# Kernel tuning notes

Hardware: AMD Instinct MI355X
Metric: run time of the kernel (lower is better)

## Reference

```python
import jax, jax.numpy as jnp
import numpy as np

N_LVL = 127.0   # 8-bit symmetric: 2**(8-1) - 1
BN_EPS = 1e-5
PATCH = 16


def quant_act(x):
    """Per-tensor 8-bit symmetric quant-dequant (HAWQ-style QuantAct, dynamic range)."""
    scale = jnp.max(jnp.abs(x)) / N_LVL
    xq = jnp.clip(jnp.round(x / scale), -N_LVL, N_LVL) * scale
    return xq, scale


def setup_inputs() -> dict:
    key = jax.random.key(0)
    k0, k1, k2, k3, k4 = jax.random.split(key, 5)
    B, C, H = 128, 3, 224
    dim = 768
    x = jax.random.normal(k0, (B, C, H, H), jnp.float32)
    W = jax.random.normal(k1, (dim, C, PATCH, PATCH), jnp.float32) * 0.02
    b = jax.random.normal(k2, (dim,), jnp.float32) * 0.02
    gamma = jnp.ones((dim,), jnp.float32)
    beta = jnp.zeros((dim,), jnp.float32)
    run_mean = jax.random.normal(k3, (dim,), jnp.float32) * 0.1
    run_var = jax.random.uniform(k4, (dim,), jnp.float32, 0.5, 1.5)
    return {"x": x, "W": W, "b": b, "gamma": gamma, "beta": beta,
            "run_mean": run_mean, "run_var": run_var}


def reference(x, W, b, gamma, beta, run_mean, run_var):
    # --- quant_input ---
    x_q, pre_s = quant_act(x)                                   # [B,3,224,224], scalar
    # --- QuantConv2d: per-out-channel 8-bit symmetric weight quant ---
    w_scale = jnp.max(jnp.abs(W), axis=(1, 2, 3), keepdims=True) / N_LVL  # [dim,1,1,1]
    w_int = jnp.round(W / w_scale)
    x_int = x_q / pre_s                                         # integer-valued activations
    comb_s = w_scale[:, 0, 0, 0] * pre_s                        # [dim] conv output scale
    b_int = jnp.round(b / comb_s)
    y = jax.lax.conv_general_dilated(
        x_int, w_int, window_strides=(PATCH, PATCH), padding='VALID',
        dimension_numbers=('NCHW', 'OIHW', 'NCHW'))             # [B,768,14,14]
    y = (y + b_int[None, :, None, None]) * comb_s[None, :, None, None]
    # --- quant_act_conv ---
    y, _ = quant_act(y)
    # --- GELU (torch nn.GELU default: exact erf) ---
    y = jax.nn.gelu(y, approximate=False)
    # --- qact1 ---
    y, _ = quant_act(y)
    # --- BatchNorm2d (eval mode, running stats) ---
    inv = gamma / jnp.sqrt(run_var + BN_EPS)
    y = y * inv[None, :, None, None] + (beta - run_mean * inv)[None, :, None, None]
    # --- qact2 ---
    y, act_scale = quant_act(y)
    return y, act_scale
```

## Files before the change

kernel.cpp:

```cpp
#include <hip/hip_runtime.h>

#define TOT   19267584
#define MROWS 25088
#define KD    768
#define NPB   196
#define CHW   150528

typedef unsigned int uint;
typedef __attribute__((ext_vector_type(4))) int i32x4;

#define OFF_AQ   0ull
#define OFF_WQ   19267584ull
#define OFF_WSC  19857408ull
#define OFF_INV  19860480ull
#define OFF_SHF  19863552ull
#define OFF_PA   19866624ull
#define OFF_PB   19871328ull
#define OFF_SC   19876032ull
#define OFF_PMN  19886880ull
#define OFF_PMX  24703776ull
#define OFF_PM2  19267584ull
#define OFF_PX2  19316736ull

__device__ __forceinline__ float wave_max(float v) {
#pragma unroll
  for (int off = 32; off > 0; off >>= 1) v = fmaxf(v, __shfl_xor(v, off));
  return v;
}

__device__ __forceinline__ float block_max(float v) {
  __shared__ float red[4];
  v = wave_max(v);
  __syncthreads();
  if ((threadIdx.x & 63) == 0) red[threadIdx.x >> 6] = v;
  __syncthreads();
  return fmaxf(fmaxf(red[0], red[1]), fmaxf(red[2], red[3]));
}

__device__ __forceinline__ size_t tiled_addr(int row, int k) {
  return (size_t)(row >> 7) * 98304 + (size_t)(k >> 6) * 8192 + ((row & 127) << 6) + (k & 63);
}

__global__ void k_max_wq(const float* __restrict__ x, float* __restrict__ pA,
                         const float* __restrict__ W, const float* __restrict__ gamma,
                         const float* __restrict__ beta, const float* __restrict__ rmean,
                         const float* __restrict__ rvar, signed char* __restrict__ wq,
                         float* __restrict__ wscale, float* __restrict__ inv_,
                         float* __restrict__ shf) {
  if (blockIdx.x < 1176) {
    const int i0 = blockIdx.x * 256 + threadIdx.x;
    const float4* x4 = (const float4*)x;
    float m = 0.f;
#pragma unroll
    for (int j = 0; j < 16; j += 4) {
      float4 a = x4[i0 + (j + 0) * 301056];
      float4 b = x4[i0 + (j + 1) * 301056];
      float4 c = x4[i0 + (j + 2) * 301056];
      float4 d = x4[i0 + (j + 3) * 301056];
      m = fmaxf(m, fmaxf(fmaxf(fabsf(a.x), fabsf(a.y)), fmaxf(fabsf(a.z), fabsf(a.w))));
      m = fmaxf(m, fmaxf(fmaxf(fabsf(b.x), fabsf(b.y)), fmaxf(fabsf(b.z), fabsf(b.w))));
      m = fmaxf(m, fmaxf(fmaxf(fabsf(c.x), fabsf(c.y)), fmaxf(fabsf(c.z), fabsf(c.w))));
      m = fmaxf(m, fmaxf(fmaxf(fabsf(d.x), fabsf(d.y)), fmaxf(fabsf(d.z), fabsf(d.w))));
    }
    float bm = block_max(m);
    if (threadIdx.x == 0) pA[blockIdx.x] = bm;
  } else {
    const int oc = blockIdx.x - 1176;
    const float* row = W + oc * KD;
    float m = 0.f;
    for (int k = threadIdx.x; k < KD; k += 256) m = fmaxf(m, fabsf(row[k]));
    const float ws_ = block_max(m) / 127.0f;
    for (int k = threadIdx.x; k < KD; k += 256)
      wq[tiled_addr(oc, k)] = (signed char)(int)rintf(row[k] / ws_);
    if (threadIdx.x == 0) {
      wscale[oc] = ws_;
      float iv = gamma[oc] / sqrtf(rvar[oc] + 1e-5f);
      inv_[oc] = iv;
      shf[oc] = __fsub_rn(beta[oc], __fmul_rn(rmean[oc], iv));
    }
  }
}

__global__ void k_im2col(const float* __restrict__ x, const float* __restrict__ pA,
                         signed char* __restrict__ aq) {
  float mm = 0.f;
  for (int i = threadIdx.x; i < 1176; i += 256) mm = fmaxf(mm, pA[i]);
  const float ps = block_max(mm) / 127.0f;
  const int u = blockIdx.x * 256 + threadIdx.x;
  const int p = u / 48, r = u - p * 48;
  const int c = r >> 4, kh = r & 15;
  const int b = p / NPB, pp = p - b * NPB;
  const int ph = pp / 14, pw = pp - ph * 14;
  const float* src = x + (((b * 3 + c) * 224 + ph * 16 + kh) * 224 + pw * 16);
  float4 v0 = *(const float4*)(src);
  float4 v1 = *(const float4*)(src + 4);
  float4 v2 = *(const float4*)(src + 8);
  float4 v3 = *(const float4*)(src + 12);
#define Q8(v) ((int)fminf(fmaxf(rintf((v) / ps), -127.f), 127.f) & 255)
  uint4 o;
  o.x = Q8(v0.x) | (Q8(v0.y) << 8) | (Q8(v0.z) << 16) | ((uint)Q8(v0.w) << 24);
  o.y = Q8(v1.x) | (Q8(v1.y) << 8) | (Q8(v1.z) << 16) | ((uint)Q8(v1.w) << 24);
  o.z = Q8(v2.x) | (Q8(v2.y) << 8) | (Q8(v2.z) << 16) | ((uint)Q8(v2.w) << 24);
  o.w = Q8(v3.x) | (Q8(v3.y) << 8) | (Q8(v3.z) << 16) | ((uint)Q8(v3.w) << 24);
#undef Q8
  *(uint4*)(aq + (size_t)(p >> 7) * 98304 + (size_t)(r >> 2) * 8192 + ((p & 127) << 6) +
            ((r & 3) << 4)) = o;
}

__device__ __forceinline__ void gl_lds16(const void* g, void* l) {
  __builtin_amdgcn_global_load_lds((const __attribute__((address_space(1))) void*)g,
                                   (__attribute__((address_space(3))) void*)l, 16, 0, 0);
}

__global__ __launch_bounds__(256) void k_gemm(const signed char* __restrict__ aq,
                                              const signed char* __restrict__ wq,
                                              const float* __restrict__ bias,
                                              const float* __restrict__ wscale,
                                              const float* __restrict__ pA,
                                              float* __restrict__ y,
                                              float* __restrict__ pB) {
  __shared__ __align__(16) signed char lA[2][8192];
  __shared__ __align__(16) signed char lB[2][8192];
  const int tid = threadIdx.x, lane = tid & 63, wv = tid >> 6;
  const int bsw = (blockIdx.x & 7) * 147 + (blockIdx.x >> 3);
  const int bm = bsw / 6, bn = bsw - 6 * (bsw / 6);
  const int wr = wv >> 1, wc = wv & 1;

  float mm = 0.f;
  for (int i = tid; i < 1176; i += 256) mm = fmaxf(mm, pA[i]);
  const float ps_ = block_max(mm) / 127.0f;

  const int ci0 = wv * 2, ci1 = wv * 2 + 1;
  const int lo = ((lane >> 2) << 6) + (((lane & 3) ^ ((lane >> 3) & 3)) << 4);
  const signed char* gA0 = aq + (size_t)bm * 98304 + ci0 * 1024 + lo;
  const signed char* gA1 = aq + (size_t)bm * 98304 + ci1 * 1024 + lo;
  const signed char* gB0 = wq + (size_t)bn * 98304 + ci0 * 1024 + lo;
  const signed char* gB1 = wq + (size_t)bn * 98304 + ci1 * 1024 + lo;

  i32x4 acc[4][4];
#pragma unroll
  for (int m = 0; m < 4; ++m)
#pragma unroll
    for (int n = 0; n < 4; ++n) acc[m][n] = (i32x4){0, 0, 0, 0};

  const int rbase = lane & 15;
  const int kg = ((lane >> 4) << 4) ^ (((lane >> 1) & 3) << 4);

#define STAGE(T, B)                                   \
  {                                                   \
    const size_t kk_ = (size_t)(T) * 8192;            \
    gl_lds16(gA0 + kk_, &lA[B][ci0 * 1024]);          \
    gl_lds16(gA1 + kk_, &lA[B][ci1 * 1024]);          \
    gl_lds16(gB0 + kk_, &lB[B][ci0 * 1024]);          \
    gl_lds16(gB1 + kk_, &lB[B][ci1 * 1024]);          \
  }

  STAGE(0, 0)
  __syncthreads();

  int cur = 0;
  for (int t = 0; t < 12; ++t) {
    if (t < 11) STAGE(t + 1, cur ^ 1)
    i32x4 af[4], bfr[4];
#pragma unroll
    for (int m = 0; m < 4; ++m)
      af[m] = *(const i32x4*)&lA[cur][(wr * 64 + m * 16 + rbase) * 64 + kg];
#pragma unroll
    for (int n = 0; n < 4; ++n)
      bfr[n] = *(const i32x4*)&lB[cur][(wc * 64 + n * 16 + rbase) * 64 + kg];
#pragma unroll
    for (int m = 0; m < 4; ++m)
#pragma unroll
      for (int n = 0; n < 4; ++n)
        acc[m][n] = __builtin_amdgcn_mfma_i32_16x16x64_i8(bfr[n], af[m], acc[m][n], 0, 0, 0);
    __syncthreads();
    cur ^= 1;
  }
#undef STAGE

  float lmax = 0.f;
#pragma unroll
  for (int n = 0; n < 4; ++n) {
    const int ocb = bn * 128 + wc * 64 + n * 16 + ((lane >> 4) << 2);
    const float4 ws4 = *(const float4*)&wscale[ocb];
    const float4 b4 = *(const float4*)&bias[ocb];
    const float c0 = ws4.x * ps_, c1 = ws4.y * ps_, c2 = ws4.z * ps_, c3 = ws4.w * ps_;
    const float i0 = rintf(b4.x / c0), i1 = rintf(b4.y / c1);
    const float i2 = rintf(b4.z / c2), i3 = rintf(b4.w / c3);
#pragma unroll
    for (int m = 0; m < 4; ++m) {
      const int p = bm * 128 + wr * 64 + m * 16 + rbase;
      float4 o;
      o.x = ((float)acc[m][n][0] + i0) * c0;
      o.y = ((float)acc[m][n][1] + i1) * c1;
      o.z = ((float)acc[m][n][2] + i2) * c2;
      o.w = ((float)acc[m][n][3] + i3) * c3;
      lmax = fmaxf(lmax, fmaxf(fmaxf(fabsf(o.x), fabsf(o.y)), fmaxf(fabsf(o.z), fabsf(o.w))));
      *(float4*)(y + (size_t)p * 768 + ocb) = o;
    }
  }
  float bm_ = block_max(lmax);
  if (tid == 0) pB[blockIdx.x] = bm_;
}

__global__ void k_gelu(const float* __restrict__ y, const float* __restrict__ pB,
                       signed char* __restrict__ k1, float* __restrict__ pmn,
                       float* __restrict__ pmx) {
  const int b = blockIdx.x;
  const int t = threadIdx.x;
  __shared__ float red[3];
  __shared__ float tab[255];
  float mm = 0.f;
  for (int i = t; i < 1176; i += 192) mm = fmaxf(mm, pB[i]);
  mm = wave_max(mm);
  __syncthreads();
  if ((t & 63) == 0) red[t >> 6] = mm;
  __syncthreads();
  const float s1 = fmaxf(fmaxf(red[0], red[1]), red[2]) / 127.0f;
  for (int i = t; i < 255; i += 192) {
    float y1 = (float)(i - 127) * s1;
    float e = erff(y1 * 0.70710678118654752f);
    tab[i] = (y1 * (e + 1.0f)) * 0.5f;
  }
  __syncthreads();
  float mn0 = 1e30f, mx0 = -1e30f, mn1 = 1e30f, mx1 = -1e30f;
  float mn2 = 1e30f, mx2 = -1e30f, mn3 = 1e30f, mx3 = -1e30f;
  const float4* y4 = (const float4*)y + (size_t)b * 16 * 192 + t;
  char4* k4 = (char4*)k1 + (size_t)b * 16 * 192 + t;
#pragma unroll 4
  for (int row = 0; row < 16; ++row) {
    float4 v = y4[row * 192];
    int a = (int)fminf(fmaxf(rintf(v.x / s1), -127.f), 127.f);
    int bq = (int)fminf(fmaxf(rintf(v.y / s1), -127.f), 127.f);
    int cq = (int)fminf(fmaxf(rintf(v.z / s1), -127.f), 127.f);
    int dq = (int)fminf(fmaxf(rintf(v.w / s1), -127.f), 127.f);
    char4 kk;
    kk.x = (signed char)a; kk.y = (signed char)bq;
    kk.z = (signed char)cq; kk.w = (signed char)dq;
    k4[row * 192] = kk;
    float g0 = tab[a + 127], g1 = tab[bq + 127], g2 = tab[cq + 127], g3 = tab[dq + 127];
    mn0 = fminf(mn0, g0); mx0 = fmaxf(mx0, g0);
    mn1 = fminf(mn1, g1); mx1 = fmaxf(mx1, g1);
    mn2 = fminf(mn2, g2); mx2 = fmaxf(mx2, g2);
    mn3 = fminf(mn3, g3); mx3 = fmaxf(mx3, g3);
  }
  float4 omn, omx;
  omn.x = mn0; omn.y = mn1; omn.z = mn2; omn.w = mn3;
  omx.x = mx0; omx.y = mx1; omx.z = mx2; omx.w = mx3;
  ((float4*)pmn)[(size_t)b * 192 + t] = omn;
  ((float4*)pmx)[(size_t)b * 192 + t] = omx;
}

__global__ void k_chred(const float* __restrict__ pmn, const float* __restrict__ pmx,
                        float* __restrict__ pm2, float* __restrict__ px2) {
  const int cg = blockIdx.x % 12, rc = blockIdx.x / 12;
  const int lane = threadIdx.x & 63, wv = threadIdx.x >> 6;
  const int c = cg * 64 + lane;
  float lo = 1e30f, hi = -1e30f;
  for (int i = wv; i < 98; i += 4) {
    const size_t a = (size_t)(rc * 98 + i) * 768 + c;
    lo = fminf(lo, pmn[a]);
    hi = fmaxf(hi, pmx[a]);
  }
  __shared__ float smn[4][64], smx[4][64];
  smn[wv][lane] = lo;
  smx[wv][lane] = hi;
  __syncthreads();
  if (threadIdx.x < 64) {
    float l = fminf(fminf(smn[0][lane], smn[1][lane]), fminf(smn[2][lane], smn[3][lane]));
    float h = fmaxf(fmaxf(smx[0][lane], smx[1][lane]), fmaxf(smx[2][lane], smx[3][lane]));
    pm2[rc * 768 + c] = l;
    px2[rc * 768 + c] = h;
  }
}

__global__ void k_scales(const float* __restrict__ pB, const float* __restrict__ pm2,
                         const float* __restrict__ px2, const float* __restrict__ inv_,
                         const float* __restrict__ shf, uint* __restrict__ sc) {
  const int t = threadIdx.x;
  float m = 0.f;
  for (int i = t; i < 1176; i += 256) m = fmaxf(m, pB[i]);
  const float s1 = block_max(m) / 127.0f;
  float cmn[3], cmx[3];
  float m2 = 0.f;
#pragma unroll
  for (int ci = 0; ci < 3; ++ci) {
    const int c = t + ci * 256;
    float mn = 1e30f, mx = -1e30f;
#pragma unroll
    for (int r = 0; r < 16; ++r) {
      mn = fminf(mn, pm2[r * 768 + c]);
      mx = fmaxf(mx, px2[r * 768 + c]);
    }
    cmn[ci] = mn;
    cmx[ci] = mx;
    m2 = fmaxf(m2, fmaxf(fabsf(mn), fabsf(mx)));
  }
  const float s2 = block_max(m2) / 127.0f;
  float m4 = 0.f;
#pragma unroll
  for (int ci = 0; ci < 3; ++ci) {
    const int c = t + ci * 256;
    float iv = inv_[c], sh = shf[c];
    float a = fminf(fmaxf(rintf(cmn[ci] / s2), -127.f), 127.f) * s2;
    float b = fminf(fmaxf(rintf(cmx[ci] / s2), -127.f), 127.f) * s2;
    float ya = __fadd_rn(__fmul_rn(a, iv), sh);
    float yb = __fadd_rn(__fmul_rn(b, iv), sh);
    m4 = fmaxf(m4, fmaxf(fabsf(ya), fabsf(yb)));
  }
  const float s3 = block_max(m4) / 127.0f;
  if (t == 0) {
    sc[0] = __float_as_uint(s1);
    sc[1] = __float_as_uint(s2);
    sc[2] = __float_as_uint(s3);
  }
}

__global__ __launch_bounds__(256) void k_final(const signed char* __restrict__ k1,
                                               const uint* __restrict__ sc,
                                               const float* __restrict__ inv_,
                                               const float* __restrict__ shf,
                                               float* __restrict__ out) {
  __shared__ signed char ks[49 * 772];
  __shared__ float tab[255];
  const float s1 = __uint_as_float(sc[0]);
  const float s2 = __uint_as_float(sc[1]);
  const float s3 = __uint_as_float(sc[2]);
  const int t = threadIdx.x;
  for (int i = t; i < 255; i += 256) {
    float y1 = (float)(i - 127) * s1;
    float e = erff(y1 * 0.70710678118654752f);
    float y2 = (y1 * (e + 1.0f)) * 0.5f;
    float q2 = fminf(fmaxf(rintf(y2 / s2), -127.f), 127.f);
    tab[i] = q2 * s2;
  }
  const int img = blockIdx.x >> 2, ch = blockIdx.x & 3;
  const int q0 = ch * 49;
  const uint4* src = (const uint4*)(k1 + (size_t)img * 150528 + (size_t)q0 * 768);
  for (int i = t; i < 2352; i += 256) {
    uint4 v = src[i];
    const int q = i / 48, r = i - q * 48;
    *(uint4*)&ks[q * 772 + r * 16] = v;
  }
  __syncthreads();
  const int lane = t & 63, wv = t >> 6;
  float* ob = out + (size_t)img * CHW + q0 + lane;
  if (lane < 49) {
    const signed char* kcol = &ks[lane * 772];
    for (int j = 0; j < 192; ++j) {
      const int oc = wv * 192 + j;
      const float iv = inv_[oc], sh = shf[oc];
      const int a = kcol[oc];
      const float f = __fadd_rn(__fmul_rn(tab[a + 127], iv), sh);
      ob[(size_t)oc * 196] = fminf(fmaxf(rintf(f / s3), -127.f), 127.f) * s3;
    }
  }
  if (blockIdx.x == 0 && t == 0) out[TOT] = s3;
}

extern "C" void kernel_launch(void* const* d_in, const int* in_sizes, int n_in,
                              void* d_out, int out_size, void* d_ws, size_t ws_size,
                              hipStream_t stream) {
  const float* x     = (const float*)d_in[0];
  const float* W     = (const float*)d_in[1];
  const float* bias  = (const float*)d_in[2];
  const float* gamma = (const float*)d_in[3];
  const float* beta  = (const float*)d_in[4];
  const float* rmean = (const float*)d_in[5];
  const float* rvar  = (const float*)d_in[6];
  float* out = (float*)d_out;
  char* ws = (char*)d_ws;

  signed char* aq  = (signed char*)(ws + OFF_AQ);
  signed char* wq  = (signed char*)(ws + OFF_WQ);
  float* wsc  = (float*)(ws + OFF_WSC);
  float* inv_ = (float*)(ws + OFF_INV);
  float* shf  = (float*)(ws + OFF_SHF);
  float* pA   = (float*)(ws + OFF_PA);
  float* pB   = (float*)(ws + OFF_PB);
  uint*  sc   = (uint*)(ws + OFF_SC);
  float* pmn  = (float*)(ws + OFF_PMN);
  float* pmx  = (float*)(ws + OFF_PMX);
  float* pm2  = (float*)(ws + OFF_PM2);
  float* px2  = (float*)(ws + OFF_PX2);
  signed char* k1 = (signed char*)(ws + OFF_AQ);

  k_max_wq<<<1944, 256, 0, stream>>>(x, pA, W, gamma, beta, rmean, rvar, wq, wsc, inv_, shf);
  k_im2col<<<4704, 256, 0, stream>>>(x, pA, aq);
  k_gemm<<<1176, 256, 0, stream>>>(aq, wq, bias, wsc, pA, out, pB);
  k_gelu<<<1568, 192, 0, stream>>>(out, pB, k1, pmn, pmx);
  k_chred<<<192, 256, 0, stream>>>(pmn, pmx, pm2, px2);
  k_scales<<<1, 256, 0, stream>>>(pB, pm2, px2, inv_, shf, sc);
  k_final<<<512, 256, 0, stream>>>(k1, sc, inv_, shf, out);
}
```

Measured before the change: 140.0 us.

## Triple-buffer GEMM LDS pipeline and pass input scale from im2col

The int8 GEMM moves from a two-stage to a three-stage global-to-LDS pipeline. It uses explicit vmcnt waits and a single barrier per k-step, so loads stay two stages ahead of the MFMA work. The GEMM also reads the input quantization scale from a workspace slot written by im2col, instead of re-reducing 1176 partial maxima in every block. LDS usage grows, which may reduce occupancy, and correctness relies on the hand-written waitcnt counts.

```diff
diff --git a/kernel.cpp b/kernel.cpp
--- a/kernel.cpp
+++ b/kernel.cpp
@@ -82,10 +82,11 @@
 }
 
 __global__ void k_im2col(const float* __restrict__ x, const float* __restrict__ pA,
-                         signed char* __restrict__ aq) {
+                         signed char* __restrict__ aq, uint* __restrict__ sc) {
   float mm = 0.f;
   for (int i = threadIdx.x; i < 1176; i += 256) mm = fmaxf(mm, pA[i]);
   const float ps = block_max(mm) / 127.0f;
+  if (blockIdx.x == 0 && threadIdx.x == 0) sc[3] = __float_as_uint(ps);
   const int u = blockIdx.x * 256 + threadIdx.x;
   const int p = u / 48, r = u - p * 48;
   const int c = r >> 4, kh = r & 15;
@@ -116,19 +117,16 @@
                                               const signed char* __restrict__ wq,
                                               const float* __restrict__ bias,
                                               const float* __restrict__ wscale,
-                                              const float* __restrict__ pA,
+                                              const uint* __restrict__ sc,
                                               float* __restrict__ y,
                                               float* __restrict__ pB) {
-  __shared__ __align__(16) signed char lA[2][8192];
-  __shared__ __align__(16) signed char lB[2][8192];
+  __shared__ __align__(16) signed char lA[3][8192];
+  __shared__ __align__(16) signed char lB[3][8192];
   const int tid = threadIdx.x, lane = tid & 63, wv = tid >> 6;
   const int bsw = (blockIdx.x & 7) * 147 + (blockIdx.x >> 3);
   const int bm = bsw / 6, bn = bsw - 6 * (bsw / 6);
   const int wr = wv >> 1, wc = wv & 1;
-
-  float mm = 0.f;
-  for (int i = tid; i < 1176; i += 256) mm = fmaxf(mm, pA[i]);
-  const float ps_ = block_max(mm) / 127.0f;
+  const float ps_ = __uint_as_float(sc[3]);
 
   const int ci0 = wv * 2, ci1 = wv * 2 + 1;
   const int lo = ((lane >> 2) << 6) + (((lane & 3) ^ ((lane >> 3) & 3)) << 4);
@@ -156,25 +154,27 @@
   }
 
   STAGE(0, 0)
-  __syncthreads();
-
-  int cur = 0;
+  STAGE(1, 1)
+#pragma unroll
   for (int t = 0; t < 12; ++t) {
-    if (t < 11) STAGE(t + 1, cur ^ 1)
+    if (t < 11) { asm volatile("s_waitcnt vmcnt(4)" ::: "memory"); }
+    else        { asm volatile("s_waitcnt vmcnt(0)" ::: "memory"); }
+    __builtin_amdgcn_s_barrier();
+    __builtin_amdgcn_sched_barrier(0);
+    const int b = t % 3;
     i32x4 af[4], bfr[4];
 #pragma unroll
     for (int m = 0; m < 4; ++m)
-      af[m] = *(const i32x4*)&lA[cur][(wr * 64 + m * 16 + rbase) * 64 + kg];
+      af[m] = *(const i32x4*)&lA[b][(wr * 64 + m * 16 + rbase) * 64 + kg];
 #pragma unroll
     for (int n = 0; n < 4; ++n)
-      bfr[n] = *(const i32x4*)&lB[cur][(wc * 64 + n * 16 + rbase) * 64 + kg];
+      bfr[n] = *(const i32x4*)&lB[b][(wc * 64 + n * 16 + rbase) * 64 + kg];
+    if (t < 10) STAGE(t + 2, (t + 2) % 3)
 #pragma unroll
     for (int m = 0; m < 4; ++m)
 #pragma unroll
       for (int n = 0; n < 4; ++n)
         acc[m][n] = __builtin_amdgcn_mfma_i32_16x16x64_i8(bfr[n], af[m], acc[m][n], 0, 0, 0);
-    __syncthreads();
-    cur ^= 1;
   }
 #undef STAGE
 
@@ -386,8 +386,8 @@
   signed char* k1 = (signed char*)(ws + OFF_AQ);
 
   k_max_wq<<<1944, 256, 0, stream>>>(x, pA, W, gamma, beta, rmean, rvar, wq, wsc, inv_, shf);
-  k_im2col<<<4704, 256, 0, stream>>>(x, pA, aq);
-  k_gemm<<<1176, 256, 0, stream>>>(aq, wq, bias, wsc, pA, out, pB);
+  k_im2col<<<4704, 256, 0, stream>>>(x, pA, aq, sc);
+  k_gemm<<<1176, 256, 0, stream>>>(aq, wq, bias, wsc, sc, out, pB);
   k_gelu<<<1568, 192, 0, stream>>>(out, pB, k1, pmn, pmx);
   k_chred<<<192, 256, 0, stream>>>(pmn, pmx, pm2, px2);
   k_scales<<<1, 256, 0, stream>>>(pB, pm2, px2, inv_, shf, sc);
```

Result: no change. 140.3 us (+0.2%).

## Recompute GEMM twice to avoid fp32 intermediate round-trip; fuse GELU quant into GEMM

Applied to the files above, without the earlier changes.

The conv GEMM is split into two passes. The first pass only computes the global abs-max of the conv output. The second pass recomputes the GEMM and directly emits the int8 quantized activations plus per-channel GELU min/max, replacing the separate GELU kernel. This removes the 77MB fp32 write and re-read of the intermediate output at the cost of running the int8 GEMM twice. The activation scale is now broadcast through a scalar slot, and the channel reduction sizes are adjusted for the new partial layout.

```diff
diff --git a/kernel.cpp b/kernel.cpp
--- a/kernel.cpp
+++ b/kernel.cpp
@@ -17,10 +17,11 @@
 #define OFF_PA   19866624ull
 #define OFF_PB   19871328ull
 #define OFF_SC   19876032ull
-#define OFF_PMN  19886880ull
-#define OFF_PMX  24703776ull
-#define OFF_PM2  19267584ull
-#define OFF_PX2  19316736ull
+#define OFF_K1   19876864ull
+#define OFF_PMN  39144448ull
+#define OFF_PMX  39746560ull
+#define OFF_PM2  40348672ull
+#define OFF_PX2  40391680ull
 
 __device__ __forceinline__ float wave_max(float v) {
 #pragma unroll
@@ -82,10 +83,11 @@
 }
 
 __global__ void k_im2col(const float* __restrict__ x, const float* __restrict__ pA,
-                         signed char* __restrict__ aq) {
+                         signed char* __restrict__ aq, uint* __restrict__ sc) {
   float mm = 0.f;
   for (int i = threadIdx.x; i < 1176; i += 256) mm = fmaxf(mm, pA[i]);
   const float ps = block_max(mm) / 127.0f;
+  if (blockIdx.x == 0 && threadIdx.x == 0) sc[3] = __float_as_uint(ps);
   const int u = blockIdx.x * 256 + threadIdx.x;
   const int p = u / 48, r = u - p * 48;
   const int c = r >> 4, kh = r & 15;
@@ -112,23 +114,18 @@
                                    (__attribute__((address_space(3))) void*)l, 16, 0, 0);
 }
 
-__global__ __launch_bounds__(256) void k_gemm(const signed char* __restrict__ aq,
-                                              const signed char* __restrict__ wq,
-                                              const float* __restrict__ bias,
-                                              const float* __restrict__ wscale,
-                                              const float* __restrict__ pA,
-                                              float* __restrict__ y,
-                                              float* __restrict__ pB) {
+__global__ __launch_bounds__(256) void k_gemm_max(const signed char* __restrict__ aq,
+                                                  const signed char* __restrict__ wq,
+                                                  const float* __restrict__ bias,
+                                                  const float* __restrict__ wscale,
+                                                  const uint* __restrict__ sc,
+                                                  float* __restrict__ pB) {
   __shared__ __align__(16) signed char lA[2][8192];
   __shared__ __align__(16) signed char lB[2][8192];
   const int tid = threadIdx.x, lane = tid & 63, wv = tid >> 6;
   const int bsw = (blockIdx.x & 7) * 147 + (blockIdx.x >> 3);
   const int bm = bsw / 6, bn = bsw - 6 * (bsw / 6);
   const int wr = wv >> 1, wc = wv & 1;
-
-  float mm = 0.f;
-  for (int i = tid; i < 1176; i += 256) mm = fmaxf(mm, pA[i]);
-  const float ps_ = block_max(mm) / 127.0f;
 
   const int ci0 = wv * 2, ci1 = wv * 2 + 1;
   const int lo = ((lane >> 2) << 6) + (((lane & 3) ^ ((lane >> 3) & 3)) << 4);
@@ -154,10 +151,8 @@
     gl_lds16(gB0 + kk_, &lB[B][ci0 * 1024]);          \
     gl_lds16(gB1 + kk_, &lB[B][ci1 * 1024]);          \
   }
-
   STAGE(0, 0)
   __syncthreads();
-
   int cur = 0;
   for (int t = 0; t < 12; ++t) {
     if (t < 11) STAGE(t + 1, cur ^ 1)
@@ -178,6 +173,7 @@
   }
 #undef STAGE
 
+  const float ps_ = __uint_as_float(sc[3]);
   float lmax = 0.f;
 #pragma unroll
   for (int n = 0; n < 4; ++n) {
@@ -189,66 +185,146 @@
     const float i2 = rintf(b4.z / c2), i3 = rintf(b4.w / c3);
 #pragma unroll
     for (int m = 0; m < 4; ++m) {
-      const int p = bm * 128 + wr * 64 + m * 16 + rbase;
-      float4 o;
-      o.x = ((float)acc[m][n][0] + i0) * c0;
-      o.y = ((float)acc[m][n][1] + i1) * c1;
-      o.z = ((float)acc[m][n][2] + i2) * c2;
-      o.w = ((float)acc[m][n][3] + i3) * c3;
-      lmax = fmaxf(lmax, fmaxf(fmaxf(fabsf(o.x), fabsf(o.y)), fmaxf(fabsf(o.z), fabsf(o.w))));
-      *(float4*)(y + (size_t)p * 768 + ocb) = o;
+      float ox = ((float)acc[m][n][0] + i0) * c0;
+      float oy = ((float)acc[m][n][1] + i1) * c1;
+      float oz = ((float)acc[m][n][2] + i2) * c2;
+      float ow = ((float)acc[m][n][3] + i3) * c3;
+      lmax = fmaxf(lmax, fmaxf(fmaxf(fabsf(ox), fabsf(oy)), fmaxf(fabsf(oz), fabsf(ow))));
     }
   }
   float bm_ = block_max(lmax);
   if (tid == 0) pB[blockIdx.x] = bm_;
 }
 
-__global__ void k_gelu(const float* __restrict__ y, const float* __restrict__ pB,
-                       signed char* __restrict__ k1, float* __restrict__ pmn,
-                       float* __restrict__ pmx) {
-  const int b = blockIdx.x;
-  const int t = threadIdx.x;
-  __shared__ float red[3];
+__global__ __launch_bounds__(256) void k_gemm_k1(const signed char* __restrict__ aq,
+                                                 const signed char* __restrict__ wq,
+                                                 const float* __restrict__ bias,
+                                                 const float* __restrict__ wscale,
+                                                 const uint* __restrict__ sc,
+                                                 const float* __restrict__ pB,
+                                                 signed char* __restrict__ k1,
+                                                 float* __restrict__ pmn,
+                                                 float* __restrict__ pmx) {
+  __shared__ __align__(16) signed char lA[2][8192];
+  __shared__ __align__(16) signed char lB[2][8192];
   __shared__ float tab[255];
+  __shared__ float smnf[2][2][4][4][4], smxf[2][2][4][4][4];
+  const int tid = threadIdx.x, lane = tid & 63, wv = tid >> 6;
+  const int bsw = (blockIdx.x & 7) * 147 + (blockIdx.x >> 3);
+  const int bm = bsw / 6, bn = bsw - 6 * (bsw / 6);
+  const int wr = wv >> 1, wc = wv & 1;
+
   float mm = 0.f;
-  for (int i = t; i < 1176; i += 192) mm = fmaxf(mm, pB[i]);
-  mm = wave_max(mm);
-  __syncthreads();
-  if ((t & 63) == 0) red[t >> 6] = mm;
-  __syncthreads();
-  const float s1 = fmaxf(fmaxf(red[0], red[1]), red[2]) / 127.0f;
-  for (int i = t; i < 255; i += 192) {
+  for (int i = tid; i < 1176; i += 256) mm = fmaxf(mm, pB[i]);
+  const float s1 = block_max(mm) / 127.0f;
+  for (int i = tid; i < 255; i += 256) {
     float y1 = (float)(i - 127) * s1;
     float e = erff(y1 * 0.70710678118654752f);
     tab[i] = (y1 * (e + 1.0f)) * 0.5f;
   }
-  __syncthreads();
-  float mn0 = 1e30f, mx0 = -1e30f, mn1 = 1e30f, mx1 = -1e30f;
-  float mn2 = 1e30f, mx2 = -1e30f, mn3 = 1e30f, mx3 = -1e30f;
-  const float4* y4 = (const float4*)y + (size_t)b * 16 * 192 + t;
-  char4* k4 = (char4*)k1 + (size_t)b * 16 * 192 + t;
-#pragma unroll 4
-  for (int row = 0; row < 16; ++row) {
-    float4 v = y4[row * 192];
-    int a = (int)fminf(fmaxf(rintf(v.x / s1), -127.f), 127.f);
-    int bq = (int)fminf(fmaxf(rintf(v.y / s1), -127.f), 127.f);
-    int cq = (int)fminf(fmaxf(rintf(v.z / s1), -127.f), 127.f);
-    int dq = (int)fminf(fmaxf(rintf(v.w / s1), -127.f), 127.f);
-    char4 kk;
-    kk.x = (signed char)a; kk.y = (signed char)bq;
-    kk.z = (signed char)cq; kk.w = (signed char)dq;
-    k4[row * 192] = kk;
-    float g0 = tab[a + 127], g1 = tab[bq + 127], g2 = tab[cq + 127], g3 = tab[dq + 127];
-    mn0 = fminf(mn0, g0); mx0 = fmaxf(mx0, g0);
-    mn1 = fminf(mn1, g1); mx1 = fmaxf(mx1, g1);
-    mn2 = fminf(mn2, g2); mx2 = fmaxf(mx2, g2);
-    mn3 = fminf(mn3, g3); mx3 = fmaxf(mx3, g3);
-  }
-  float4 omn, omx;
-  omn.x = mn0; omn.y = mn1; omn.z = mn2; omn.w = mn3;
-  omx.x = mx0; omx.y = mx1; omx.z = mx2; omx.w = mx3;
-  ((float4*)pmn)[(size_t)b * 192 + t] = omn;
-  ((float4*)pmx)[(size_t)b * 192 + t] = omx;
+
+  const int ci0 = wv * 2, ci1 = wv * 2 + 1;
+  const int lo = ((lane >> 2) << 6) + (((lane & 3) ^ ((lane >> 3) & 3)) << 4);
+  const signed char* gA0 = aq + (size_t)bm * 98304 + ci0 * 1024 + lo;
+  const signed char* gA1 = aq + (size_t)bm * 98304 + ci1 * 1024 + lo;
+  const signed char* gB0 = wq + (size_t)bn * 98304 + ci0 * 1024 + lo;
+  const signed char* gB1 = wq + (size_t)bn * 98304 + ci1 * 1024 + lo;
+
+  i32x4 acc[4][4];
+#pragma unroll
+  for (int m = 0; m < 4; ++m)
+#pragma unroll
+    for (int n = 0; n < 4; ++n) acc[m][n] = (i32x4){0, 0, 0, 0};
+
+  const int rbase = lane & 15;
+  const int kg = ((lane >> 4) << 4) ^ (((lane >> 1) & 3) << 4);
+
+#define STAGE(T, B)                                   \
+  {                                                   \
+    const size_t kk_ = (size_t)(T) * 8192;            \
+    gl_lds16(gA0 + kk_, &lA[B][ci0 * 1024]);          \
+    gl_lds16(gA1 + kk_, &lA[B][ci1 * 1024]);          \
+    gl_lds16(gB0 + kk_, &lB[B][ci0 * 1024]);          \
+    gl_lds16(gB1 + kk_, &lB[B][ci1 * 1024]);          \
+  }
+  STAGE(0, 0)
+  __syncthreads();
+  int cur = 0;
+  for (int t = 0; t < 12; ++t) {
+    if (t < 11) STAGE(t + 1, cur ^ 1)
+    i32x4 af[4], bfr[4];
+#pragma unroll
+    for (int m = 0; m < 4; ++m)
+      af[m] = *(const i32x4*)&lA[cur][(wr * 64 + m * 16 + rbase) * 64 + kg];
+#pragma unroll
+    for (int n = 0; n < 4; ++n)
+      bfr[n] = *(const i32x4*)&lB[cur][(wc * 64 + n * 16 + rbase) * 64 + kg];
+#pragma unroll
+    for (int m = 0; m < 4; ++m)
+#pragma unroll
+      for (int n = 0; n < 4; ++n)
+        acc[m][n] = __builtin_amdgcn_mfma_i32_16x16x64_i8(bfr[n], af[m], acc[m][n], 0, 0, 0);
+    __syncthreads();
+    cur ^= 1;
+  }
+#undef STAGE
+
+  const float ps_ = __uint_as_float(sc[3]);
+  const int g = lane >> 4;
+#pragma unroll
+  for (int n = 0; n < 4; ++n) {
+    const int ocb = bn * 128 + wc * 64 + n * 16 + (g << 2);
+    const float4 ws4 = *(const float4*)&wscale[ocb];
+    const float4 b4 = *(const float4*)&bias[ocb];
+    const float c0 = ws4.x * ps_, c1 = ws4.y * ps_, c2 = ws4.z * ps_, c3 = ws4.w * ps_;
+    const float i0 = rintf(b4.x / c0), i1 = rintf(b4.y / c1);
+    const float i2 = rintf(b4.z / c2), i3 = rintf(b4.w / c3);
+    float jmn0 = 1e30f, jmn1 = 1e30f, jmn2 = 1e30f, jmn3 = 1e30f;
+    float jmx0 = -1e30f, jmx1 = -1e30f, jmx2 = -1e30f, jmx3 = -1e30f;
+#pragma unroll
+    for (int m = 0; m < 4; ++m) {
+      const int p = bm * 128 + wr * 64 + m * 16 + rbase;
+      float ox = ((float)acc[m][n][0] + i0) * c0;
+      float oy = ((float)acc[m][n][1] + i1) * c1;
+      float oz = ((float)acc[m][n][2] + i2) * c2;
+      float ow = ((float)acc[m][n][3] + i3) * c3;
+      int q0 = (int)fminf(fmaxf(rintf(ox / s1), -127.f), 127.f);
+      int q1 = (int)fminf(fmaxf(rintf(oy / s1), -127.f), 127.f);
+      int q2 = (int)fminf(fmaxf(rintf(oz / s1), -127.f), 127.f);
+      int q3 = (int)fminf(fmaxf(rintf(ow / s1), -127.f), 127.f);
+      char4 kk;
+      kk.x = (signed char)q0; kk.y = (signed char)q1;
+      kk.z = (signed char)q2; kk.w = (signed char)q3;
+      *(char4*)(k1 + (size_t)p * 768 + ocb) = kk;
+      float g0 = tab[q0 + 127], g1 = tab[q1 + 127], g2 = tab[q2 + 127], g3 = tab[q3 + 127];
+      jmn0 = fminf(jmn0, g0); jmx0 = fmaxf(jmx0, g0);
+      jmn1 = fminf(jmn1, g1); jmx1 = fmaxf(jmx1, g1);
+      jmn2 = fminf(jmn2, g2); jmx2 = fmaxf(jmx2, g2);
+      jmn3 = fminf(jmn3, g3); jmx3 = fmaxf(jmx3, g3);
+    }
+#pragma unroll
+    for (int off = 1; off < 16; off <<= 1) {
+      jmn0 = fminf(jmn0, __shfl_xor(jmn0, off)); jmx0 = fmaxf(jmx0, __shfl_xor(jmx0, off));
+      jmn1 = fminf(jmn1, __shfl_xor(jmn1, off)); jmx1 = fmaxf(jmx1, __shfl_xor(jmx1, off));
+      jmn2 = fminf(jmn2, __shfl_xor(jmn2, off)); jmx2 = fmaxf(jmx2, __shfl_xor(jmx2, off));
+      jmn3 = fminf(jmn3, __shfl_xor(jmn3, off)); jmx3 = fmaxf(jmx3, __shfl_xor(jmx3, off));
+    }
+    if (rbase == 0) {
+      smnf[wr][wc][n][g][0] = jmn0; smnf[wr][wc][n][g][1] = jmn1;
+      smnf[wr][wc][n][g][2] = jmn2; smnf[wr][wc][n][g][3] = jmn3;
+      smxf[wr][wc][n][g][0] = jmx0; smxf[wr][wc][n][g][1] = jmx1;
+      smxf[wr][wc][n][g][2] = jmx2; smxf[wr][wc][n][g][3] = jmx3;
+    }
+  }
+  __syncthreads();
+  if (tid < 128) {
+    const int wcc = tid >> 6, r = tid & 63;
+    const int nn = r >> 4, gg = (r >> 2) & 3, jj = tid & 3;
+    float mn = fminf(smnf[0][wcc][nn][gg][jj], smnf[1][wcc][nn][gg][jj]);
+    float mx = fmaxf(smxf[0][wcc][nn][gg][jj], smxf[1][wcc][nn][gg][jj]);
+    pmn[(size_t)bm * 768 + bn * 128 + tid] = mn;
+    pmx[(size_t)bm * 768 + bn * 128 + tid] = mx;
+  }
 }
 
 __global__ void k_chred(const float* __restrict__ pmn, const float* __restrict__ pmx,
@@ -257,8 +333,8 @@
   const int lane = threadIdx.x & 63, wv = threadIdx.x >> 6;
   const int c = cg * 64 + lane;
   float lo = 1e30f, hi = -1e30f;
-  for (int i = wv; i < 98; i += 4) {
-    const size_t a = (size_t)(rc * 98 + i) * 768 + c;
+  for (int i = wv; i < 14; i += 4) {
+    const size_t a = (size_t)(rc * 14 + i) * 768 + c;
     lo = fminf(lo, pmn[a]);
     hi = fmaxf(hi, pmx[a]);
   }
@@ -288,7 +364,7 @@
     const int c = t + ci * 256;
     float mn = 1e30f, mx = -1e30f;
 #pragma unroll
-    for (int r = 0; r < 16; ++r) {
+    for (int r = 0; r < 14; ++r) {
       mn = fminf(mn, pm2[r * 768 + c]);
       mx = fmaxf(mx, px2[r * 768 + c]);
     }
@@ -379,17 +455,17 @@
   float* pA   = (float*)(ws + OFF_PA);
   float* pB   = (float*)(ws + OFF_PB);
   uint*  sc   = (uint*)(ws + OFF_SC);
+  signed char* k1 = (signed char*)(ws + OFF_K1);
   float* pmn  = (float*)(ws + OFF_PMN);
   float* pmx  = (float*)(ws + OFF_PMX);
   float* pm2  = (float*)(ws + OFF_PM2);
   float* px2  = (float*)(ws + OFF_PX2);
-  signed char* k1 = (signed char*)(ws + OFF_AQ);
 
   k_max_wq<<<1944, 256, 0, stream>>>(x, pA, W, gamma, beta, rmean, rvar, wq, wsc, inv_, shf);
-  k_im2col<<<4704, 256, 0, stream>>>(x, pA, aq);
-  k_gemm<<<1176, 256, 0, stream>>>(aq, wq, bias, wsc, pA, out, pB);
-  k_gelu<<<1568, 192, 0, stream>>>(out, pB, k1, pmn, pmx);
-  k_chred<<<192, 256, 0, stream>>>(pmn, pmx, pm2, px2);
+  k_im2col<<<4704, 256, 0, stream>>>(x, pA, aq, sc);
+  k_gemm_max<<<1176, 256, 0, stream>>>(aq, wq, bias, wsc, sc, pB);
+  k_gemm_k1<<<1176, 256, 0, stream>>>(aq, wq, bias, wsc, sc, pB, k1, pmn, pmx);
+  k_chred<<<168, 256, 0, stream>>>(pmn, pmx, pm2, px2);
   k_scales<<<1, 256, 0, stream>>>(pB, pm2, px2, inv_, shf, sc);
   k_final<<<512, 256, 0, stream>>>(k1, sc, inv_, shf, out);
 }
```

Result: no change. 137.2 us (-2.0%).
